# Optimization experiments

Measured on AMD Instinct MI355X. Metric: run time of the kernel, lower is better.

Reference implementation:

```python
import jax, jax.numpy as jnp
import numpy as np

MATCH_TIMES = 4  # init kwarg match_times


def box_xyxy_to_cxcywh(x):
    # x: [..., 4] in (x0, y0, x1, y1)
    x0, y0, x1, y1 = jnp.split(x, 4, axis=-1)
    return jnp.concatenate([(x0 + x1) * 0.5, (y0 + y1) * 0.5, x1 - x0, y1 - y0], axis=-1)


def _pairwise_l1(a, b):
    # a: [B, Q, 4], b: [B, T, 4] -> [B, Q, T] L1 cost matrix
    return jnp.sum(jnp.abs(a[:, :, None, :] - b[:, None, :, :]), axis=-1)


def setup_inputs() -> dict:
    key = jax.random.key(0)
    k1, k2, k3 = jax.random.split(key, 3)
    B, Q, T = 8, 32768, 64
    pred_boxes = jax.random.uniform(k1, (B, Q, 4), dtype=jnp.float32)
    anchors = jax.random.uniform(k2, (B, Q, 4), dtype=jnp.float32)
    gt_boxes = jax.random.uniform(k3, (B, T, 4), dtype=jnp.float32)
    return {"pred_boxes": pred_boxes, "anchors": anchors, "gt_boxes": gt_boxes}


def reference(pred_boxes, anchors, gt_boxes):
    B, Q = pred_boxes.shape[:2]
    T = gt_boxes.shape[1]
    mt = MATCH_TIMES

    gt_c = box_xyxy_to_cxcywh(gt_boxes)
    C = _pairwise_l1(box_xyxy_to_cxcywh(pred_boxes), gt_c)   # [B, Q, T]
    C1 = _pairwise_l1(box_xyxy_to_cxcywh(anchors), gt_c)     # [B, Q, T]

    # per-target k SMALLEST-cost query indices (topk(largest=False))
    _, idx = jax.lax.top_k(-jnp.swapaxes(C, 1, 2), mt)    # [B, T, mt]
    _, idx1 = jax.lax.top_k(-jnp.swapaxes(C1, 1, 2), mt)  # [B, T, mt]

    # per target: concat pred-based and anchor-based matches, then hstack over targets
    idx_i = jnp.concatenate([idx, idx1], axis=-1).reshape(B, T * 2 * mt).astype(jnp.int64)
    # per target j-indices: range(mt) twice (as in source), tiled over targets
    j_row = jnp.tile(jnp.concatenate([jnp.arange(mt), jnp.arange(mt)]), T)  # [T*2*mt]
    idx_j = jnp.broadcast_to(j_row, (B, T * 2 * mt)).astype(jnp.int64)
    return idx_i, idx_j
```

## Files before the change

kernel.cpp:

```cpp
#include <hip/hip_runtime.h>
#include <float.h>

constexpr int Bn = 8, Qn = 32768, Tn = 64, MT = 4;
constexpr int BLOCK = 256;
constexpr int CHUNKS = 64;
constexpr int CHUNK  = Qn / CHUNKS;
constexpr int PARTS  = BLOCK / 64;
constexpr int SUB    = CHUNK / PARTS;

__device__ __forceinline__ void cmpx(float& av, int& ai, float& bv, int& bi) {
    bool sw = (bv < av) || ((bv == av) && (bi < ai));
    float v0 = sw ? bv : av; int i0 = sw ? bi : ai;
    float v1 = sw ? av : bv; int i1 = sw ? ai : bi;
    av = v0; ai = i0; bv = v1; bi = i1;
}

__device__ __forceinline__ void merge4(float a_v[4], int a_i[4],
                                       const float b_v[4], const int b_i[4]) {
    float mv[4]; int mi[4];
#pragma unroll
    for (int k = 0; k < 4; ++k) {
        float bv = b_v[3 - k]; int bi = b_i[3 - k];
        bool ta = (a_v[k] < bv) || ((a_v[k] == bv) && (a_i[k] < bi));
        mv[k] = ta ? a_v[k] : bv;
        mi[k] = ta ? a_i[k] : bi;
    }
    cmpx(mv[0], mi[0], mv[2], mi[2]);
    cmpx(mv[1], mi[1], mv[3], mi[3]);
    cmpx(mv[0], mi[0], mv[1], mi[1]);
    cmpx(mv[2], mi[2], mv[3], mi[3]);
#pragma unroll
    for (int k = 0; k < 4; ++k) { a_v[k] = mv[k]; a_i[k] = mi[k]; }
}

__global__ __launch_bounds__(BLOCK) void matcher_stage1(
        const float* __restrict__ pred, const float* __restrict__ anch,
        const float* __restrict__ gt, float2* __restrict__ partial) {
    const int c     = blockIdx.x;
    const int which = blockIdx.y;
    const int b     = blockIdx.z;
    const int tid   = threadIdx.x;

    __shared__ float4 sbox[CHUNK];
    __shared__ float2 sred[PARTS][64][4];

    const float4* bp = (const float4*)((which ? anch : pred) + (size_t)b * Qn * 4)
                       + (size_t)c * CHUNK;
#pragma unroll
    for (int i = tid; i < CHUNK; i += BLOCK) {
        float4 p = bp[i];
        sbox[i] = make_float4((p.x + p.z) * 0.5f, (p.y + p.w) * 0.5f,
                              p.z - p.x, p.w - p.y);
    }

    const int t    = tid & 63;
    const int part = tid >> 6;
    const float4 g = *(const float4*)(gt + ((size_t)b * Tn + t) * 4);
    const float gcx = (g.x + g.z) * 0.5f;
    const float gcy = (g.y + g.w) * 0.5f;
    const float gw  = g.z - g.x;
    const float gh  = g.w - g.y;

    __syncthreads();

    float v[4]  = {FLT_MAX, FLT_MAX, FLT_MAX, FLT_MAX};
    int   ix[4] = {0x7fffffff, 0x7fffffff, 0x7fffffff, 0x7fffffff};

    const int j0 = part * SUB;
    const int qbase = c * CHUNK + j0;
#pragma unroll 4
    for (int jj = 0; jj < SUB; ++jj) {
        float4 p = sbox[j0 + jj];
        float cst = fabsf(p.x - gcx) + fabsf(p.y - gcy);
        cst += fabsf(p.z - gw);
        cst += fabsf(p.w - gh);
        const int q = qbase + jj;
        bool b3 = cst < v[3], b2 = cst < v[2], b1 = cst < v[1], b0 = cst < v[0];
        v[3] = b2 ? v[2] : (b3 ? cst : v[3]);  ix[3] = b2 ? ix[2] : (b3 ? q : ix[3]);
        v[2] = b1 ? v[1] : (b2 ? cst : v[2]);  ix[2] = b1 ? ix[1] : (b2 ? q : ix[2]);
        v[1] = b0 ? v[0] : (b1 ? cst : v[1]);  ix[1] = b0 ? ix[0] : (b1 ? q : ix[1]);
        v[0] = b0 ? cst : v[0];                ix[0] = b0 ? q    : ix[0];
    }

#pragma unroll
    for (int k = 0; k < 4; ++k)
        sred[part][t][k] = make_float2(v[k], __int_as_float(ix[k]));
    __syncthreads();

    if (tid < 64) {
#pragma unroll
        for (int p2 = 1; p2 < PARTS; ++p2) {
            float bv[4]; int bi[4];
#pragma unroll
            for (int k = 0; k < 4; ++k) {
                float2 e = sred[p2][t][k];
                bv[k] = e.x; bi[k] = __float_as_int(e.y);
            }
            merge4(v, ix, bv, bi);
        }
        const int bw = b * 2 + which;
        float2* dst = partial + (((size_t)bw * 64 + t) * CHUNKS + c) * 4;
#pragma unroll
        for (int k = 0; k < 4; ++k)
            dst[k] = make_float2(v[k], __int_as_float(ix[k]));
    }
}

__global__ __launch_bounds__(BLOCK) void matcher_stage2(
        const float2* __restrict__ partial,
        int* __restrict__ out_i, int* __restrict__ out_j) {
    const int lane = threadIdx.x & 63;
    const int gwv  = blockIdx.x * (BLOCK / 64) + (threadIdx.x >> 6);
    const int bw = gwv >> 6;
    const int t  = gwv & 63;

    const float2* src = partial + (((size_t)bw * 64 + t) * CHUNKS + lane) * 4;
    float v[4]; int ix[4];
#pragma unroll
    for (int k = 0; k < 4; ++k) {
        float2 e = src[k];
        v[k] = e.x; ix[k] = __float_as_int(e.y);
    }
#pragma unroll
    for (int d = 1; d < 64; d <<= 1) {
        float bv[4]; int bi[4];
#pragma unroll
        for (int k = 0; k < 4; ++k) {
            bv[k] = __shfl_xor(v[k], d, 64);
            bi[k] = __shfl_xor(ix[k], d, 64);
        }
        merge4(v, ix, bv, bi);
    }
    if (lane == 0) {
        const int b = bw >> 1, which = bw & 1;
        const int base = ((b * Tn + t) * 2 + which) * MT;
#pragma unroll
        for (int k = 0; k < 4; ++k) {
            out_i[base + k] = ix[k];
            out_j[base + k] = k;
        }
    }
}

extern "C" void kernel_launch(void* const* d_in, const int* in_sizes, int n_in,
                              void* d_out, int out_size, void* d_ws, size_t ws_size,
                              hipStream_t stream) {
    const float* pred = (const float*)d_in[0];
    const float* anch = (const float*)d_in[1];
    const float* gt   = (const float*)d_in[2];
    int* out = (int*)d_out;
    float2* partial = (float2*)d_ws;
    const int half = Bn * Tn * 2 * MT;

    dim3 grid1(CHUNKS, 2, Bn);
    matcher_stage1<<<grid1, BLOCK, 0, stream>>>(pred, anch, gt, partial);

    const int tuples = Bn * 2 * Tn;
    dim3 grid2(tuples / (BLOCK / 64));
    matcher_stage2<<<grid2, BLOCK, 0, stream>>>(partial, out, out + half);
}
```

Before: 86.01 us.

## Use fmed3 top-4 insertion, pad reduction smem, and transpose partial layout

Rewrites the per-query top-4 insertion so the value updates use fminf and AMD fmed3 instead of compare/select chains, keeping the selects only for indices. Raises the inner loop unroll from 4 to 8 and pads the shared reduction buffer to avoid LDS bank conflicts. Reorders the partial workspace layout to chunk-major and has stage 2 read it with two float4 loads. The stage-2 reads become strided across lanes, which may hurt coalescing, and the larger unroll raises register pressure.

```diff
diff --git a/kernel.cpp b/kernel.cpp
--- a/kernel.cpp
+++ b/kernel.cpp
@@ -42,7 +42,7 @@
     const int tid   = threadIdx.x;
 
     __shared__ float4 sbox[CHUNK];
-    __shared__ float2 sred[PARTS][64][4];
+    __shared__ float2 sred[PARTS][64][5];
 
     const float4* bp = (const float4*)((which ? anch : pred) + (size_t)b * Qn * 4)
                        + (size_t)c * CHUNK;
@@ -68,18 +68,25 @@
 
     const int j0 = part * SUB;
     const int qbase = c * CHUNK + j0;
-#pragma unroll 4
+#pragma unroll 8
     for (int jj = 0; jj < SUB; ++jj) {
         float4 p = sbox[j0 + jj];
-        float cst = fabsf(p.x - gcx) + fabsf(p.y - gcy);
-        cst += fabsf(p.z - gw);
-        cst += fabsf(p.w - gh);
+        float d0 = p.x - gcx, d1 = p.y - gcy, d2 = p.z - gw, d3 = p.w - gh;
+        float cst = fabsf(d0) + fabsf(d1);
+        cst += fabsf(d2);
+        cst += fabsf(d3);
         const int q = qbase + jj;
-        bool b3 = cst < v[3], b2 = cst < v[2], b1 = cst < v[1], b0 = cst < v[0];
-        v[3] = b2 ? v[2] : (b3 ? cst : v[3]);  ix[3] = b2 ? ix[2] : (b3 ? q : ix[3]);
-        v[2] = b1 ? v[1] : (b2 ? cst : v[2]);  ix[2] = b1 ? ix[1] : (b2 ? q : ix[2]);
-        v[1] = b0 ? v[0] : (b1 ? cst : v[1]);  ix[1] = b0 ? ix[0] : (b1 ? q : ix[1]);
-        v[0] = b0 ? cst : v[0];                ix[0] = b0 ? q    : ix[0];
+        float n0 = fminf(v[0], cst);
+        float n1 = __builtin_amdgcn_fmed3f(v[0], v[1], cst);
+        float n2 = __builtin_amdgcn_fmed3f(v[1], v[2], cst);
+        float n3 = __builtin_amdgcn_fmed3f(v[2], v[3], cst);
+        bool b0 = cst < v[0], b1 = cst < v[1], b2 = cst < v[2], b3 = cst < v[3];
+        int i3 = b2 ? ix[2] : (b3 ? q : ix[3]);
+        int i2 = b1 ? ix[1] : (b2 ? q : ix[2]);
+        int i1 = b0 ? ix[0] : (b1 ? q : ix[1]);
+        int i0 = b0 ? q : ix[0];
+        v[0] = n0; v[1] = n1; v[2] = n2; v[3] = n3;
+        ix[0] = i0; ix[1] = i1; ix[2] = i2; ix[3] = i3;
     }
 
 #pragma unroll
@@ -99,7 +106,7 @@
             merge4(v, ix, bv, bi);
         }
         const int bw = b * 2 + which;
-        float2* dst = partial + (((size_t)bw * 64 + t) * CHUNKS + c) * 4;
+        float2* dst = partial + (((size_t)bw * CHUNKS + c) * 64 + t) * 4;
 #pragma unroll
         for (int k = 0; k < 4; ++k)
             dst[k] = make_float2(v[k], __int_as_float(ix[k]));
@@ -114,13 +121,14 @@
     const int bw = gwv >> 6;
     const int t  = gwv & 63;
 
-    const float2* src = partial + (((size_t)bw * 64 + t) * CHUNKS + lane) * 4;
+    const float4* src4 = (const float4*)(partial + (((size_t)bw * CHUNKS + lane) * 64 + t) * 4);
+    float4 e0 = src4[0], e1 = src4[1];
     float v[4]; int ix[4];
-#pragma unroll
-    for (int k = 0; k < 4; ++k) {
-        float2 e = src[k];
-        v[k] = e.x; ix[k] = __float_as_int(e.y);
-    }
+    v[0] = e0.x; ix[0] = __float_as_int(e0.y);
+    v[1] = e0.z; ix[1] = __float_as_int(e0.w);
+    v[2] = e1.x; ix[2] = __float_as_int(e1.y);
+    v[3] = e1.z; ix[3] = __float_as_int(e1.w);
+
 #pragma unroll
     for (int d = 1; d < 64; d <<= 1) {
         float bv[4]; int bi[4];
```

After: 83.02 us (median of 2 runs). 1.04x faster.
